# Kernel optimization log

Hardware: AMD Instinct MI355X
Metric: run time of the kernel (lower is better)

Reference implementation:

```python
import jax, jax.numpy as jnp
import numpy as np

B, T, C = 4, 2048, 1024
H, DH = 16, 64  # head_count, per-head dim = head_size // head_count


def setup_inputs() -> dict:
    key = jax.random.key(0)
    ks = jax.random.split(key, 5)
    s = 1.0 / np.sqrt(C)
    return {
        "x": jax.random.normal(ks[0], (B, T, C), dtype=jnp.float32),
        "Wq": jax.random.normal(ks[1], (H, C, DH), dtype=jnp.float32) * s,
        "Wk": jax.random.normal(ks[2], (H, C, DH), dtype=jnp.float32) * s,
        "Wv": jax.random.normal(ks[3], (H, C, DH), dtype=jnp.float32) * s,
        "Wproj": jax.random.normal(ks[4], (C, C), dtype=jnp.float32) * s,
    }


def reference(x, Wq, Wk, Wv, Wproj):
    b, t, c = x.shape
    q = jnp.einsum("btc,hcd->bhtd", x, Wq)
    k = jnp.einsum("btc,hcd->bhtd", x, Wk)
    v = jnp.einsum("btc,hcd->bhtd", x, Wv)
    # NOTE: source scales by embed_size**-0.5, not head_dim**-0.5
    wei = jnp.einsum("bhtd,bhsd->bhts", q, k) * (c ** -0.5)
    causal = jnp.tril(jnp.ones((t, t), dtype=bool))
    wei = jnp.where(causal, wei, jnp.finfo(wei.dtype).min)
    wei = jax.nn.softmax(wei, axis=-1)
    out = jnp.einsum("bhts,bhsd->bhtd", wei, v)
    out = out.transpose(0, 2, 1, 3).reshape(b, t, -1)  # concat heads -> [B,T,H*DH]
    return out @ Wproj
```

## Files before the change

### kernel.cpp

```cpp
#include <hip/hip_runtime.h>
#include <math.h>
#include <stdint.h>

#define BB 4
#define TT 2048
#define CC 1024
#define HH 16
#define DH 64
#define BT (BB*TT)
#define NQKV (3*HH*DH)

typedef __attribute__((ext_vector_type(8))) __bf16 bf16x8;
typedef __attribute__((ext_vector_type(4))) float f32x4;
typedef __attribute__((ext_vector_type(16))) float f32x16;
typedef __attribute__((ext_vector_type(8))) unsigned short u16x8;
typedef __attribute__((ext_vector_type(4))) unsigned short u16x4;
typedef __attribute__((ext_vector_type(4))) unsigned int u32x4;

__device__ __forceinline__ unsigned short f2b(float f) {
  union { float f; unsigned u; } v; v.f = f;
  unsigned r = v.u + 0x7fffu + ((v.u >> 16) & 1u);
  return (unsigned short)(r >> 16);
}

__device__ __forceinline__ void gload_lds16(const void* g, void* lds) {
  __builtin_amdgcn_global_load_lds(
      (const __attribute__((address_space(1))) void*)(uintptr_t)g,
      (__attribute__((address_space(3))) void*)(uintptr_t)lds, 16, 0, 0);
}

__device__ __forceinline__ unsigned cvtpk_bf16(float lo, float hi) {
  unsigned r;
  asm("v_cvt_pk_bf16_f32 %0, %1, %2" : "=v"(r) : "v"(lo), "v"(hi));
  return r;
}

__device__ __forceinline__ float fexp2(float x) {
#if __has_builtin(__builtin_amdgcn_exp2f)
  return __builtin_amdgcn_exp2f(x);
#else
  float r; asm("v_exp_f32 %0, %1" : "=v"(r) : "v"(x)); return r;
#endif
}

__global__ __launch_bounds__(256) void cvt_bf16(const float* __restrict__ in,
                                                unsigned short* __restrict__ out, int n) {
  int i = (blockIdx.x * 256 + threadIdx.x) * 8;
  if (i + 8 > n) return;
  float4 a = *(const float4*)(in + i);
  float4 b = *(const float4*)(in + i + 4);
  u16x8 pk;
  pk[0] = f2b(a.x); pk[1] = f2b(a.y); pk[2] = f2b(a.z); pk[3] = f2b(a.w);
  pk[4] = f2b(b.x); pk[5] = f2b(b.y); pk[6] = f2b(b.z); pk[7] = f2b(b.w);
  *(u16x8*)(out + i) = pk;
}

__global__ __launch_bounds__(256) void transpose_cvt_qkv(
    const float* __restrict__ Wq, const float* __restrict__ Wk, const float* __restrict__ Wv,
    unsigned short* __restrict__ out) {
  __shared__ float tile[32][33];
  const int z = blockIdx.z;
  const float* in = (z < 16 ? Wq : (z < 32 ? Wk : Wv)) + (size_t)(z & 15) * CC * DH;
  unsigned short* o = out + (size_t)z * CC * DH;
  const int r0 = blockIdx.y * 32, c0 = blockIdx.x * 32;
  const int tx = threadIdx.x, ty = threadIdx.y;
  #pragma unroll
  for (int i = 0; i < 32; i += 8)
    tile[ty + i][tx] = in[(size_t)(r0 + ty + i) * DH + c0 + tx];
  __syncthreads();
  #pragma unroll
  for (int i = 0; i < 32; i += 8)
    o[(size_t)(c0 + ty + i) * CC + r0 + tx] = f2b(tile[tx][ty + i]);
}

__global__ __launch_bounds__(256) void transpose_cvt(const float* __restrict__ in,
                                                     unsigned short* __restrict__ out,
                                                     int R, int Cc) {
  __shared__ float tile[32][33];
  const int r0 = blockIdx.y * 32, c0 = blockIdx.x * 32;
  const int tx = threadIdx.x, ty = threadIdx.y;
  #pragma unroll
  for (int i = 0; i < 32; i += 8)
    tile[ty + i][tx] = in[(size_t)(r0 + ty + i) * Cc + c0 + tx];
  __syncthreads();
  #pragma unroll
  for (int i = 0; i < 32; i += 8)
    out[(size_t)(c0 + ty + i) * R + r0 + tx] = f2b(tile[tx][ty + i]);
}

template<int MODE>
__global__ __launch_bounds__(256) void mfma_gemm(
    const unsigned short* __restrict__ A,
    const unsigned short* __restrict__ Bt,
    void* __restrict__ Cout, unsigned short* __restrict__ VTout,
    int M, int N, int K)
{
  __shared__ unsigned short As[2 * 128 * 64];
  __shared__ unsigned short Bs[2 * 128 * 64];
  const int tid = threadIdx.x;
  const int l = tid & 63, w = tid >> 6;
  const int wr = w >> 1, wc = w & 1;

  const int wid = blockIdx.y * gridDim.x + blockIdx.x;
  const int local = wid >> 3;
  const int rt = (wid & 7) * 8 + (local & 7);
  const int ct = local >> 3;
  const long row0 = (long)rt * 128, col0 = (long)ct * 128;

  const bool SWAP = (MODE == 1) || (ct < 16);

  const int srowA = w * 32 + (l >> 3);
  const int schunk = (l & 7) ^ ((l >> 3) & 7);
  const unsigned short* Ap = A + (row0 + srowA) * (long)K + schunk * 8;
  const unsigned short* Bp = Bt + (col0 + srowA) * (long)K + schunk * 8;
  const size_t woff = (size_t)w * 4096;

  f32x4 acc[4][4];
  #pragma unroll
  for (int i = 0; i < 4; ++i)
    #pragma unroll
    for (int j = 0; j < 4; ++j) acc[i][j] = (f32x4){0.f, 0.f, 0.f, 0.f};

  const int fr = l & 15, fg = l >> 4;
  const int fswz = fr & 7;

  #pragma unroll
  for (int i = 0; i < 4; ++i) {
    gload_lds16(Ap + (size_t)i * 8 * K, (char*)As + woff + i * 1024);
    gload_lds16(Bp + (size_t)i * 8 * K, (char*)Bs + woff + i * 1024);
  }
  __syncthreads();

  const int NT = K >> 6;
  for (int kt = 0; kt < NT; ++kt) {
    const int cur = kt & 1;
    if (kt + 1 < NT) {
      const long k0 = (long)(kt + 1) * 64;
      char* Ad = (char*)As + (cur ^ 1) * 16384 + woff;
      char* Bd = (char*)Bs + (cur ^ 1) * 16384 + woff;
      #pragma unroll
      for (int i = 0; i < 4; ++i) {
        gload_lds16(Ap + (size_t)i * 8 * K + k0, Ad + i * 1024);
        gload_lds16(Bp + (size_t)i * 8 * K + k0, Bd + i * 1024);
      }
    }
    const char* aB = (const char*)As + cur * 16384;
    const char* bB = (const char*)Bs + cur * 16384;
    #pragma unroll
    for (int kk = 0; kk < 2; ++kk) {
      bf16x8 af[4], bfr[4];
      #pragma unroll
      for (int m = 0; m < 4; ++m)
        af[m] = *(const bf16x8*)(aB + (wr * 64 + m * 16 + fr) * 128 + (((fg + kk * 4) ^ fswz) << 4));
      #pragma unroll
      for (int n = 0; n < 4; ++n)
        bfr[n] = *(const bf16x8*)(bB + (wc * 64 + n * 16 + fr) * 128 + (((fg + kk * 4) ^ fswz) << 4));
      if (SWAP) {
        #pragma unroll
        for (int m = 0; m < 4; ++m)
          #pragma unroll
          for (int n = 0; n < 4; ++n)
            acc[m][n] = __builtin_amdgcn_mfma_f32_16x16x32_bf16(bfr[n], af[m], acc[m][n], 0, 0, 0);
      } else {
        #pragma unroll
        for (int m = 0; m < 4; ++m)
          #pragma unroll
          for (int n = 0; n < 4; ++n)
            acc[m][n] = __builtin_amdgcn_mfma_f32_16x16x32_bf16(af[m], bfr[n], acc[m][n], 0, 0, 0);
      }
    }
    __syncthreads();
  }

  const int fq = l >> 4;
  if (MODE == 1) {
    #pragma unroll
    for (int m = 0; m < 4; ++m) {
      long grow = row0 + wr * 64 + m * 16 + fr;
      #pragma unroll
      for (int n = 0; n < 4; ++n) {
        long gcol0 = col0 + wc * 64 + n * 16 + fq * 4;
        float4 v = make_float4(acc[m][n][0], acc[m][n][1], acc[m][n][2], acc[m][n][3]);
        *(float4*)&((float*)Cout)[grow * (long)N + gcol0] = v;
      }
    }
  } else if (ct < 16) {
    #pragma unroll
    for (int m = 0; m < 4; ++m) {
      int t = (int)(row0 + wr * 64 + m * 16 + fr);
      int b = t >> 11, tt = t & 2047;
      #pragma unroll
      for (int n = 0; n < 4; ++n) {
        long gcol0 = col0 + wc * 64 + n * 16 + fq * 4;
        int which = (int)(gcol0 >> 10);
        int h = (int)((gcol0 >> 6) & 15);
        int d0 = (int)(gcol0 & 63);
        float sc = (which == 0) ? 0.04508422017f : 1.f;
        u16x4 pk;
        #pragma unroll
        for (int r = 0; r < 4; ++r) pk[r] = f2b(acc[m][n][r] * sc);
        *(u16x4*)&((unsigned short*)Cout)[((((size_t)which * BB + b) * HH + h) * TT + tt) * DH + d0] = pk;
      }
    }
  } else {
    #pragma unroll
    for (int m = 0; m < 4; ++m) {
      long grow0 = row0 + wr * 64 + m * 16 + fq * 4;
      int b = (int)(grow0 >> 11), t0 = (int)(grow0 & 2047);
      #pragma unroll
      for (int n = 0; n < 4; ++n) {
        long gcol = col0 + wc * 64 + n * 16 + fr;
        int h = (int)((gcol >> 6) & 15);
        int d = (int)(gcol & 63);
        u16x4 pk;
        #pragma unroll
        for (int r = 0; r < 4; ++r) pk[r] = f2b(acc[m][n][r]);
        *(u16x4*)&VTout[((size_t)(b * HH + h) * DH + d) * TT + t0] = pk;
      }
    }
  }
}

__device__ __forceinline__ int crow(int r, int hi) { return (r & 3) + 8 * (r >> 2) + 4 * hi; }

__device__ __forceinline__ void swap32(unsigned a, unsigned b, int hi,
                                       unsigned& L, unsigned& H) {
#if __has_builtin(__builtin_amdgcn_permlane32_swap)
  typedef unsigned uint2v __attribute__((ext_vector_type(2)));
  uint2v rr = __builtin_amdgcn_permlane32_swap(a, b, false, false);
  L = rr[0]; H = rr[1];
#else
  unsigned ax = __shfl_xor((int)a, 32, 64), bx = __shfl_xor((int)b, 32, 64);
  L = hi ? bx : a;
  H = hi ? b : ax;
#endif
}

__device__ __forceinline__ void sm_nomax(const f32x16& s, bool diag, int lq, int hi,
                                         float& lsum, bf16x8& pf0, bf16x8& pf1) {
  float p[16];
  #pragma unroll
  for (int r = 0; r < 16; ++r) {
    float e = fexp2(fminf(s[r], 80.f));
    if (diag && (crow(r, hi) > lq)) e = 0.f;
    p[r] = e;
  }
  float t[8];
  #pragma unroll
  for (int r = 0; r < 8; ++r) t[r] = p[r] + p[r + 8];
  #pragma unroll
  for (int r = 0; r < 4; ++r) t[r] = t[r] + t[r + 4];
  lsum += ((t[0] + t[1]) + (t[2] + t[3]));

  unsigned U[4][2];
  #pragma unroll
  for (int g = 0; g < 4; ++g) {
    U[g][0] = cvtpk_bf16(p[4 * g + 0], p[4 * g + 1]);
    U[g][1] = cvtpk_bf16(p[4 * g + 2], p[4 * g + 3]);
  }
  unsigned L0, H0, L1, H1;
  swap32(U[0][0], U[1][0], hi, L0, H0);
  swap32(U[0][1], U[1][1], hi, L1, H1);
  pf0 = __builtin_bit_cast(bf16x8, (u32x4){L0, L1, H0, H1});
  swap32(U[2][0], U[3][0], hi, L0, H0);
  swap32(U[2][1], U[3][1], hi, L1, H1);
  pf1 = __builtin_bit_cast(bf16x8, (u32x4){L0, L1, H0, H1});
}

__global__ __launch_bounds__(256, 2) void attn_mfma(
    const unsigned short* __restrict__ Qb, const unsigned short* __restrict__ Kb,
    const unsigned short* __restrict__ VTb, unsigned short* __restrict__ Ob)
{
  __shared__ unsigned short Ksm[64 * 64];
  __shared__ unsigned short VTsm[64 * 64];

  const int bh = blockIdx.x;
  const int bx = blockIdx.y;
  const int b = bh >> 4, h = bh & 15;
  const int tid = threadIdx.x;
  const int w = tid >> 6, lane = tid & 63;
  const int lq = lane & 31, hi = lane >> 5;
  const int qa0 = bx * 128 + w * 32;
  const int qb0 = (15 - bx) * 128 + w * 32;
  const int ta = qa0 + lq, tb = qb0 + lq;

  const unsigned short* Kp  = Kb  + (size_t)bh * TT * DH;
  const unsigned short* VTp = VTb + (size_t)bh * DH * TT;

  bf16x8 qfa[4], qfb[4];
  {
    const unsigned short* qpa = Qb + ((size_t)bh * TT + ta) * DH + hi * 8;
    const unsigned short* qpb = Qb + ((size_t)bh * TT + tb) * DH + hi * 8;
    #pragma unroll
    for (int c = 0; c < 4; ++c) {
      qfa[c] = *(const bf16x8*)(qpa + c * 16);
      qfb[c] = *(const bf16x8*)(qpb + c * 16);
    }
  }

  f32x16 accA[2], accB[2];
  #pragma unroll
  for (int dt = 0; dt < 2; ++dt)
    #pragma unroll
    for (int r = 0; r < 16; ++r) { accA[dt][r] = 0.f; accB[dt][r] = 0.f; }
  float lsA = 0.f, lsB = 0.f;

  char* Kc = (char*)Ksm;
  char* Vc = (char*)VTsm;

  const int srow_in = (lane >> 3);
  const int schunk = (lane & 7) ^ (srow_in & 7);
  const int sdoff = w * 2048 + lane * 16;

  const int ntiles = (15 - bx) * 2 + 2;
  for (int tile = 0; tile < ntiles; ++tile) {
    const int kv0 = tile * 64;
    __syncthreads();
    {
      const unsigned short* kg = Kp + (size_t)(kv0 + w * 16 + srow_in) * DH + schunk * 8;
      gload_lds16(kg, Kc + sdoff);
      gload_lds16(kg + 8 * DH, Kc + sdoff + 1024);
      const unsigned short* vg = VTp + (size_t)(w * 16 + srow_in) * TT + kv0 + schunk * 8;
      gload_lds16(vg, Vc + sdoff);
      gload_lds16(vg + 8 * TT, Vc + sdoff + 1024);
    }
    __syncthreads();

    #pragma unroll
    for (int sub = 0; sub < 2; ++sub) {
      const int ks = kv0 + sub * 32;
      if (ks > qb0) break;

      const int arow = sub * 32 + lq;
      const int aswz = (arow & 7) << 4;
      bf16x8 kf[4];
      #pragma unroll
      for (int c = 0; c < 4; ++c)
        kf[c] = *(const bf16x8*)(Kc + ((arow * 128 + (c * 16 + hi * 8) * 2) ^ aswz));

      f32x16 s;
      #pragma unroll
      for (int r = 0; r < 16; ++r) s[r] = 0.f;
      __builtin_amdgcn_s_setprio(1);
      #pragma unroll
      for (int c = 0; c < 4; ++c)
        s = __builtin_amdgcn_mfma_f32_32x32x16_bf16(kf[c], qfb[c], s, 0, 0, 0);
      __builtin_amdgcn_s_setprio(0);
      bf16x8 pB0, pB1;
      sm_nomax(s, ks == qb0, lq, hi, lsB, pB0, pB1);

      const bool actA = (ks <= qa0);
      bf16x8 pA0, pA1;
      if (actA) {
        f32x16 s2;
        #pragma unroll
        for (int r = 0; r < 16; ++r) s2[r] = 0.f;
        __builtin_amdgcn_s_setprio(1);
        #pragma unroll
        for (int c = 0; c < 4; ++c)
          s2 = __builtin_amdgcn_mfma_f32_32x32x16_bf16(kf[c], qfa[c], s2, 0, 0, 0);
        __builtin_amdgcn_s_setprio(0);
        sm_nomax(s2, ks == qa0, lq, hi, lsA, pA0, pA1);
      }

      __builtin_amdgcn_s_setprio(1);
      #pragma unroll
      for (int kc = 0; kc < 2; ++kc) {
        bf16x8 pB = kc ? pB1 : pB0;
        bf16x8 pA = kc ? pA1 : pA0;
        #pragma unroll
        for (int dt = 0; dt < 2; ++dt) {
          const int vrow = dt * 32 + lq;
          bf16x8 vf = *(const bf16x8*)(Vc + ((vrow * 128 + sub * 64 + kc * 32 + hi * 16) ^ ((vrow & 7) << 4)));
          accB[dt] = __builtin_amdgcn_mfma_f32_32x32x16_bf16(vf, pB, accB[dt], 0, 0, 0);
          if (actA)
            accA[dt] = __builtin_amdgcn_mfma_f32_32x32x16_bf16(vf, pA, accA[dt], 0, 0, 0);
        }
      }
      __builtin_amdgcn_s_setprio(0);
    }
  }

  {
    const float l = lsA + __shfl_xor(lsA, 32, 64);
    const float inv = 1.f / l;
    unsigned short* op = Ob + ((size_t)b * TT + ta) * CC + h * DH;
    #pragma unroll
    for (int dt = 0; dt < 2; ++dt)
      #pragma unroll
      for (int r = 0; r < 16; ++r)
        op[dt * 32 + crow(r, hi)] = f2b(accA[dt][r] * inv);
  }
  {
    const float l = lsB + __shfl_xor(lsB, 32, 64);
    const float inv = 1.f / l;
    unsigned short* op = Ob + ((size_t)b * TT + tb) * CC + h * DH;
    #pragma unroll
    for (int dt = 0; dt < 2; ++dt)
      #pragma unroll
      for (int r = 0; r < 16; ++r)
        op[dt * 32 + crow(r, hi)] = f2b(accB[dt][r] * inv);
  }
}

extern "C" void kernel_launch(void* const* d_in, const int* in_sizes, int n_in,
                              void* d_out, int out_size, void* d_ws, size_t ws_size,
                              hipStream_t stream) {
  const float* x     = (const float*)d_in[0];
  const float* Wq    = (const float*)d_in[1];
  const float* Wk    = (const float*)d_in[2];
  const float* Wv    = (const float*)d_in[3];
  const float* Wproj = (const float*)d_in[4];

  unsigned short* xb  = (unsigned short*)d_ws;
  unsigned short* Wt  = xb + (size_t)BT * CC;
  unsigned short* WpT = Wt + (size_t)NQKV * CC;
  unsigned short* QKV = WpT + (size_t)CC * CC;
  unsigned short* Ob  = QKV + (size_t)3 * BB * HH * TT * DH;
  unsigned short* Qb  = QKV;
  unsigned short* Kb  = QKV + (size_t)BB * HH * TT * DH;
  unsigned short* VT  = Kb + (size_t)BB * HH * TT * DH;

  cvt_bf16<<<4096, 256, 0, stream>>>(x, xb, BT * CC);
  dim3 tb(32, 8);
  transpose_cvt_qkv<<<dim3(2, 32, 48), tb, 0, stream>>>(Wq, Wk, Wv, Wt);
  transpose_cvt<<<dim3(32, 32, 1), tb, 0, stream>>>(Wproj, WpT, CC, CC);

  mfma_gemm<0><<<dim3(64, 24), 256, 0, stream>>>(xb, Wt, QKV, VT, BT, NQKV, CC);
  attn_mfma<<<dim3(64, 8), 256, 0, stream>>>(Qb, Kb, VT, Ob);
  mfma_gemm<1><<<dim3(64, 8), 256, 0, stream>>>(Ob, WpT, d_out, nullptr, BT, CC, CC);
}
```

Baseline: 190.7 us.

## Double-buffer K/V tiles in LDS to overlap global loads with MFMA

The attention kernel now keeps two LDS buffers for the K and V^T tiles. It issues the async global-to-LDS loads for the next tile before computing on the current one, and uses one barrier per iteration instead of two. This hides load latency behind the QK/PV MFMA work. In exchange, LDS use per block doubles to 32KB, which could limit occupancy. Correctness also depends on the direct-to-LDS loads having completed before the trailing barrier (vmcnt wait).

```diff
diff --git a/kernel.cpp b/kernel.cpp
--- a/kernel.cpp
+++ b/kernel.cpp
@@ -271,8 +271,8 @@
     const unsigned short* __restrict__ Qb, const unsigned short* __restrict__ Kb,
     const unsigned short* __restrict__ VTb, unsigned short* __restrict__ Ob)
 {
-  __shared__ unsigned short Ksm[64 * 64];
-  __shared__ unsigned short VTsm[64 * 64];
+  __shared__ unsigned short Ksm[2 * 64 * 64];
+  __shared__ unsigned short VTsm[2 * 64 * 64];
 
   const int bh = blockIdx.x;
   const int bx = blockIdx.y;
@@ -312,19 +312,29 @@
   const int schunk = (lane & 7) ^ (srow_in & 7);
   const int sdoff = w * 2048 + lane * 16;
 
+  auto stage = [&](int tile, int buf) {
+    const unsigned short* kg = Kp + (size_t)(tile * 64 + w * 16 + srow_in) * DH + schunk * 8;
+    char* kd = Kc + buf * 8192 + sdoff;
+    gload_lds16(kg, kd);
+    gload_lds16(kg + 8 * DH, kd + 1024);
+    const unsigned short* vg = VTp + (size_t)(w * 16 + srow_in) * TT + tile * 64 + schunk * 8;
+    char* vd = Vc + buf * 8192 + sdoff;
+    gload_lds16(vg, vd);
+    gload_lds16(vg + 8 * TT, vd + 1024);
+  };
+
   const int ntiles = (15 - bx) * 2 + 2;
+
+  stage(0, 0);
+  __syncthreads();
+
   for (int tile = 0; tile < ntiles; ++tile) {
+    const int cur = tile & 1;
+    if (tile + 1 < ntiles) stage(tile + 1, cur ^ 1);
+
+    const char* Kt = Kc + cur * 8192;
+    const char* Vt = Vc + cur * 8192;
     const int kv0 = tile * 64;
-    __syncthreads();
-    {
-      const unsigned short* kg = Kp + (size_t)(kv0 + w * 16 + srow_in) * DH + schunk * 8;
-      gload_lds16(kg, Kc + sdoff);
-      gload_lds16(kg + 8 * DH, Kc + sdoff + 1024);
-      const unsigned short* vg = VTp + (size_t)(w * 16 + srow_in) * TT + kv0 + schunk * 8;
-      gload_lds16(vg, Vc + sdoff);
-      gload_lds16(vg + 8 * TT, Vc + sdoff + 1024);
-    }
-    __syncthreads();
 
     #pragma unroll
     for (int sub = 0; sub < 2; ++sub) {
@@ -336,7 +346,7 @@
       bf16x8 kf[4];
       #pragma unroll
       for (int c = 0; c < 4; ++c)
-        kf[c] = *(const bf16x8*)(Kc + ((arow * 128 + (c * 16 + hi * 8) * 2) ^ aswz));
+        kf[c] = *(const bf16x8*)(Kt + ((arow * 128 + (c * 16 + hi * 8) * 2) ^ aswz));
 
       f32x16 s;
       #pragma unroll
@@ -371,7 +381,7 @@
         #pragma unroll
         for (int dt = 0; dt < 2; ++dt) {
           const int vrow = dt * 32 + lq;
-          bf16x8 vf = *(const bf16x8*)(Vc + ((vrow * 128 + sub * 64 + kc * 32 + hi * 16) ^ ((vrow & 7) << 4)));
+          bf16x8 vf = *(const bf16x8*)(Vt + ((vrow * 128 + sub * 64 + kc * 32 + hi * 16) ^ ((vrow & 7) << 4)));
           accB[dt] = __builtin_amdgcn_mfma_f32_32x32x16_bf16(vf, pB, accB[dt], 0, 0, 0);
           if (actA)
             accA[dt] = __builtin_amdgcn_mfma_f32_32x32x16_bf16(vf, pA, accA[dt], 0, 0, 0);
@@ -379,6 +389,8 @@
       }
       __builtin_amdgcn_s_setprio(0);
     }
+
+    __syncthreads();
   }
 
   {
```

Result: no change. 192.5 us (+0.9%).

## Split paired causal query blocks into separate attention workgroups

Applied to the files above, without the earlier changes.

The attention kernel previously paired a short and a long causal query block per workgroup, sharing K/V tile loads for balance. Now each workgroup handles a single 128-row query block, launching twice as many workgroups with launch bounds raised to 4 blocks per CU. This lowers register pressure and raises occupancy and parallelism, but it loses the shared K/V loads and the built-in load balancing. Each K/V tile is therefore loaded once per workgroup rather than once per pair, and per-block work becomes uneven (scheduled longest-first via reversed blockIdx.y).

```diff
diff --git a/kernel.cpp b/kernel.cpp
--- a/kernel.cpp
+++ b/kernel.cpp
@@ -267,7 +267,7 @@
   pf1 = __builtin_bit_cast(bf16x8, (u32x4){L0, L1, H0, H1});
 }
 
-__global__ __launch_bounds__(256, 2) void attn_mfma(
+__global__ __launch_bounds__(256, 4) void attn_mfma(
     const unsigned short* __restrict__ Qb, const unsigned short* __restrict__ Kb,
     const unsigned short* __restrict__ VTb, unsigned short* __restrict__ Ob)
 {
@@ -275,35 +275,30 @@
   __shared__ unsigned short VTsm[64 * 64];
 
   const int bh = blockIdx.x;
-  const int bx = blockIdx.y;
+  const int qblk = 15 - blockIdx.y;
   const int b = bh >> 4, h = bh & 15;
   const int tid = threadIdx.x;
   const int w = tid >> 6, lane = tid & 63;
   const int lq = lane & 31, hi = lane >> 5;
-  const int qa0 = bx * 128 + w * 32;
-  const int qb0 = (15 - bx) * 128 + w * 32;
-  const int ta = qa0 + lq, tb = qb0 + lq;
+  const int qw0 = qblk * 128 + w * 32;
+  const int tq = qw0 + lq;
 
   const unsigned short* Kp  = Kb  + (size_t)bh * TT * DH;
   const unsigned short* VTp = VTb + (size_t)bh * DH * TT;
 
-  bf16x8 qfa[4], qfb[4];
+  bf16x8 qf[4];
   {
-    const unsigned short* qpa = Qb + ((size_t)bh * TT + ta) * DH + hi * 8;
-    const unsigned short* qpb = Qb + ((size_t)bh * TT + tb) * DH + hi * 8;
-    #pragma unroll
-    for (int c = 0; c < 4; ++c) {
-      qfa[c] = *(const bf16x8*)(qpa + c * 16);
-      qfb[c] = *(const bf16x8*)(qpb + c * 16);
-    }
-  }
-
-  f32x16 accA[2], accB[2];
+    const unsigned short* qp = Qb + ((size_t)bh * TT + tq) * DH + hi * 8;
+    #pragma unroll
+    for (int c = 0; c < 4; ++c) qf[c] = *(const bf16x8*)(qp + c * 16);
+  }
+
+  f32x16 acc[2];
   #pragma unroll
   for (int dt = 0; dt < 2; ++dt)
     #pragma unroll
-    for (int r = 0; r < 16; ++r) { accA[dt][r] = 0.f; accB[dt][r] = 0.f; }
-  float lsA = 0.f, lsB = 0.f;
+    for (int r = 0; r < 16; ++r) acc[dt][r] = 0.f;
+  float ls = 0.f;
 
   char* Kc = (char*)Ksm;
   char* Vc = (char*)VTsm;
@@ -312,7 +307,7 @@
   const int schunk = (lane & 7) ^ (srow_in & 7);
   const int sdoff = w * 2048 + lane * 16;
 
-  const int ntiles = (15 - bx) * 2 + 2;
+  const int ntiles = qblk * 2 + 2;
   for (int tile = 0; tile < ntiles; ++tile) {
     const int kv0 = tile * 64;
     __syncthreads();
@@ -329,7 +324,7 @@
     #pragma unroll
     for (int sub = 0; sub < 2; ++sub) {
       const int ks = kv0 + sub * 32;
-      if (ks > qb0) break;
+      if (ks > qw0) break;
 
       const int arow = sub * 32 + lq;
       const int aswz = (arow & 7) << 4;
@@ -344,37 +339,20 @@
       __builtin_amdgcn_s_setprio(1);
       #pragma unroll
       for (int c = 0; c < 4; ++c)
-        s = __builtin_amdgcn_mfma_f32_32x32x16_bf16(kf[c], qfb[c], s, 0, 0, 0);
+        s = __builtin_amdgcn_mfma_f32_32x32x16_bf16(kf[c], qf[c], s, 0, 0, 0);
       __builtin_amdgcn_s_setprio(0);
-      bf16x8 pB0, pB1;
-      sm_nomax(s, ks == qb0, lq, hi, lsB, pB0, pB1);
-
-      const bool actA = (ks <= qa0);
-      bf16x8 pA0, pA1;
-      if (actA) {
-        f32x16 s2;
-        #pragma unroll
-        for (int r = 0; r < 16; ++r) s2[r] = 0.f;
-        __builtin_amdgcn_s_setprio(1);
-        #pragma unroll
-        for (int c = 0; c < 4; ++c)
-          s2 = __builtin_amdgcn_mfma_f32_32x32x16_bf16(kf[c], qfa[c], s2, 0, 0, 0);
-        __builtin_amdgcn_s_setprio(0);
-        sm_nomax(s2, ks == qa0, lq, hi, lsA, pA0, pA1);
-      }
+      bf16x8 p0, p1;
+      sm_nomax(s, ks == qw0, lq, hi, ls, p0, p1);
 
       __builtin_amdgcn_s_setprio(1);
       #pragma unroll
       for (int kc = 0; kc < 2; ++kc) {
-        bf16x8 pB = kc ? pB1 : pB0;
-        bf16x8 pA = kc ? pA1 : pA0;
+        bf16x8 pf = kc ? p1 : p0;
         #pragma unroll
         for (int dt = 0; dt < 2; ++dt) {
           const int vrow = dt * 32 + lq;
           bf16x8 vf = *(const bf16x8*)(Vc + ((vrow * 128 + sub * 64 + kc * 32 + hi * 16) ^ ((vrow & 7) << 4)));
-          accB[dt] = __builtin_amdgcn_mfma_f32_32x32x16_bf16(vf, pB, accB[dt], 0, 0, 0);
-          if (actA)
-            accA[dt] = __builtin_amdgcn_mfma_f32_32x32x16_bf16(vf, pA, accA[dt], 0, 0, 0);
+          acc[dt] = __builtin_amdgcn_mfma_f32_32x32x16_bf16(vf, pf, acc[dt], 0, 0, 0);
         }
       }
       __builtin_amdgcn_s_setprio(0);
@@ -382,24 +360,14 @@
   }
 
   {
-    const float l = lsA + __shfl_xor(lsA, 32, 64);
+    const float l = ls + __shfl_xor(ls, 32, 64);
     const float inv = 1.f / l;
-    unsigned short* op = Ob + ((size_t)b * TT + ta) * CC + h * DH;
+    unsigned short* op = Ob + ((size_t)b * TT + tq) * CC + h * DH;
     #pragma unroll
     for (int dt = 0; dt < 2; ++dt)
       #pragma unroll
       for (int r = 0; r < 16; ++r)
-        op[dt * 32 + crow(r, hi)] = f2b(accA[dt][r] * inv);
-  }
-  {
-    const float l = lsB + __shfl_xor(lsB, 32, 64);
-    const float inv = 1.f / l;
-    unsigned short* op = Ob + ((size_t)b * TT + tb) * CC + h * DH;
-    #pragma unroll
-    for (int dt = 0; dt < 2; ++dt)
-      #pragma unroll
-      for (int r = 0; r < 16; ++r)
-        op[dt * 32 + crow(r, hi)] = f2b(accB[dt][r] * inv);
+        op[dt * 32 + crow(r, hi)] = f2b(acc[dt][r] * inv);
   }
 }
 
@@ -427,6 +395,6 @@
   transpose_cvt<<<dim3(32, 32, 1), tb, 0, stream>>>(Wproj, WpT, CC, CC);
 
   mfma_gemm<0><<<dim3(64, 24), 256, 0, stream>>>(xb, Wt, QKV, VT, BT, NQKV, CC);
-  attn_mfma<<<dim3(64, 8), 256, 0, stream>>>(Qb, Kb, VT, Ob);
+  attn_mfma<<<dim3(64, 16), 256, 0, stream>>>(Qb, Kb, VT, Ob);
   mfma_gemm<1><<<dim3(64, 8), 256, 0, stream>>>(Ob, WpT, d_out, nullptr, BT, CC, CC);
 }
```

Result: faster. 174.0 us (-8.8%).
